# Optimization experiments

Measured on AMD Instinct MI355X. Metric: run time of the kernel, lower is better.

Reference implementation:

```python
import jax, jax.numpy as jnp
import numpy as np

Q_MAX = 127.0          # 2**(8-1) - 1
QUANTILE = 0.99
GAMMA_MIN, GAMMA_MAX = 0.1, 10.0


def setup_inputs() -> dict:
    key = jax.random.key(0)
    k1, _ = jax.random.split(key)
    x = jax.random.normal(k1, (4, 4096, 2048), dtype=jnp.float32)
    gamma = jnp.ones((1,), dtype=jnp.float32)
    return {"x": x, "gamma": gamma}


def reference(x, gamma):
    # --- quantile of |x| (torch: x.flatten().abs().sort().values[k]) ---
    n = x.size
    k = int(round(QUANTILE * n))
    x_abs = jnp.abs(x.ravel())
    # faithful to full-sort-then-index (the kernel-headroom target)
    q_quantile = jax.lax.stop_gradient(jnp.sort(x_abs)[k])

    # first call: buffer initialized to q_quantile, then EMA with itself
    # -> effective running quantile == q_quantile on this step.
    gamma_c = jnp.clip(gamma, GAMMA_MIN, GAMMA_MAX)  # in-place data clamp in torch
    scale = (q_quantile / Q_MAX) * gamma_c            # shape (1,)

    # omniquant: affine fake-quantize with straight-through estimator
    xq = jnp.clip(jnp.round(x / scale), -Q_MAX - 1.0, Q_MAX) * scale
    out = x + jax.lax.stop_gradient(xq - x)           # STE
    return out
```

## Files before the change

### kernel.cpp

```cpp
#include <hip/hip_runtime.h>
#include <math.h>

typedef unsigned int u32;
typedef unsigned long long u64;
typedef float nfloat4 __attribute__((ext_vector_type(4)));

#define AL(p) __hip_atomic_load((p), __ATOMIC_RELAXED, __HIP_MEMORY_SCOPE_AGENT)


#define G1 0
#define SC 2048
#define TK 2056
#define CS 2060
#define H2 4096
#define ZERO_U32 (4096 + (1 << 20))

__global__ __launch_bounds__(1024) void hist_top(const u32* __restrict__ x,
                                                 u32* __restrict__ ws,
                                                 long long n, u32 k) {
  u32* g1 = ws + G1;
  u32* sc = ws + SC;
  __shared__ u32 h[2048 * 8];
  const int t = threadIdx.x;
  for (int i = t; i < 2048 * 8; i += 1024) h[i] = 0;
  __syncthreads();

  const u32 r = (u32)(t & 7);
  const long long n4 = n >> 2;
  const long long stride = (long long)gridDim.x * 1024;
  const uint4* x4 = (const uint4*)x;
  for (long long i = (long long)blockIdx.x * 1024 + t; i < n4; i += stride) {
    uint4 v = x4[i];
    atomicAdd(&h[(((v.x & 0x7fffffffu) >> 20) << 3) + r], 1u);
    atomicAdd(&h[(((v.y & 0x7fffffffu) >> 20) << 3) + r], 1u);
    atomicAdd(&h[(((v.z & 0x7fffffffu) >> 20) << 3) + r], 1u);
    atomicAdd(&h[(((v.w & 0x7fffffffu) >> 20) << 3) + r], 1u);
  }
  for (long long i = (n4 << 2) + (long long)blockIdx.x * 1024 + t; i < n;
       i += stride)
    atomicAdd(&h[(((x[i] & 0x7fffffffu) >> 20) << 3) + r], 1u);
  __syncthreads();
  for (int i = t; i < 2048; i += 1024) {
    u32 c = 0;
#pragma unroll
    for (int j = 0; j < 8; ++j) c += h[(i << 3) + j];
    if (c) atomicAdd(&g1[i], c);
  }
  __syncthreads();
  __shared__ u32 isLast;
  if (t == 0) {
    u32 done = __hip_atomic_fetch_add(ws + TK, 1u, __ATOMIC_ACQ_REL,
                                      __HIP_MEMORY_SCOPE_AGENT);
    isLast = (done == (u32)(gridDim.x - 1));
  }
  __syncthreads();
  if (!isLast) return;
  u32* s = h;
  const u32 c0 = AL(&g1[2 * t]);
  const u32 c1 = AL(&g1[2 * t + 1]);
  const u32 sum = c0 + c1;
  s[t] = sum;
  __syncthreads();
  for (int off = 1; off < 1024; off <<= 1) {
    u32 add = (t >= off) ? s[t - off] : 0u;
    __syncthreads();
    s[t] += add;
    __syncthreads();
  }
  u32 ex = s[t] - sum;
  if (k >= ex && k < ex + c0) { sc[0] = 2 * t; sc[1] = k - ex; }
  ex += c0;
  if (k >= ex && k < ex + c1) { sc[0] = 2 * t + 1; sc[1] = k - ex; }
}

__global__ __launch_bounds__(1024) void hist_low(const u32* __restrict__ x,
                                                 u32* __restrict__ ws,
                                                 long long n) {
  const u32 B1 = ws[SC + 0];
  u32* h2 = ws + H2;
  const int t = threadIdx.x;
  const long long n4 = n >> 2;
  const long long stride = (long long)gridDim.x * 1024;
  const uint4* x4 = (const uint4*)x;
  for (long long i = (long long)blockIdx.x * 1024 + t; i < n4; i += stride) {
    uint4 v = x4[i];
    u32 a;
    a = v.x & 0x7fffffffu; if ((a >> 20) == B1) atomicAdd(&h2[a & 0xFFFFFu], 1u);
    a = v.y & 0x7fffffffu; if ((a >> 20) == B1) atomicAdd(&h2[a & 0xFFFFFu], 1u);
    a = v.z & 0x7fffffffu; if ((a >> 20) == B1) atomicAdd(&h2[a & 0xFFFFFu], 1u);
    a = v.w & 0x7fffffffu; if ((a >> 20) == B1) atomicAdd(&h2[a & 0xFFFFFu], 1u);
  }
  for (long long i = (n4 << 2) + (long long)blockIdx.x * 1024 + t; i < n;
       i += stride) {
    u32 a = x[i] & 0x7fffffffu;
    if ((a >> 20) == B1) atomicAdd(&h2[a & 0xFFFFFu], 1u);
  }
}

__global__ __launch_bounds__(256) void chunk_fin(u32* __restrict__ ws,
                                                 const float* __restrict__ gamma) {
  const u32* h2 = ws + H2;
  u32* cs = ws + CS;
  u32* sc = ws + SC;
  const int t = threadIdx.x;
  const int b = blockIdx.x;
  uint4 v = ((const uint4*)(h2 + (size_t)b * 1024))[t];
  u32 sum = v.x + v.y + v.z + v.w;
#pragma unroll
  for (int off = 32; off > 0; off >>= 1) sum += __shfl_down(sum, off, 64);
  __shared__ u32 w[4];
  if ((t & 63) == 0) w[t >> 6] = sum;
  __syncthreads();
  __shared__ u32 isLast;
  if (t == 0) {
    const u32 total = w[0] + w[1] + w[2] + w[3];
    if (total) atomicAdd(&cs[b], total);
    u32 done = __hip_atomic_fetch_add(ws + TK + 1, 1u, __ATOMIC_ACQ_REL,
                                      __HIP_MEMORY_SCOPE_AGENT);
    isLast = (done == (u32)(gridDim.x - 1));
  }
  __syncthreads();
  if (!isLast) return;
  __shared__ u32 s[256];
  __shared__ u32 sChunk, sK2;
  const u32 k1 = sc[1];
  u32 c[4];
#pragma unroll
  for (int j = 0; j < 4; ++j) c[j] = AL(&cs[4 * t + j]);
  u32 mySum = c[0] + c[1] + c[2] + c[3];
  s[t] = mySum;
  __syncthreads();
  for (int off = 1; off < 256; off <<= 1) {
    u32 add = (t >= off) ? s[t - off] : 0u;
    __syncthreads();
    s[t] += add;
    __syncthreads();
  }
  u32 ex = s[t] - mySum;
#pragma unroll
  for (int j = 0; j < 4; ++j) {
    if (k1 >= ex && k1 < ex + c[j]) {
      sChunk = (u32)(4 * t + j);
      sK2 = k1 - ex;
    }
    ex += c[j];
  }
  __syncthreads();
  const u32 csel = sChunk;
  const u32 k2 = sK2;
  u32 c2[4];
#pragma unroll
  for (int j = 0; j < 4; ++j) c2[j] = h2[(size_t)csel * 1024 + 4 * t + j];
  mySum = c2[0] + c2[1] + c2[2] + c2[3];
  __syncthreads();
  s[t] = mySum;
  __syncthreads();
  for (int off = 1; off < 256; off <<= 1) {
    u32 add = (t >= off) ? s[t - off] : 0u;
    __syncthreads();
    s[t] += add;
    __syncthreads();
  }
  ex = s[t] - mySum;
#pragma unroll
  for (int j = 0; j < 4; ++j) {
    if (k2 >= ex && k2 < ex + c2[j]) {
      const u32 bits = (sc[0] << 20) | (csel * 1024u + (u32)(4 * t + j));
      const float q = __uint_as_float(bits);
      float gm = gamma[0];
      gm = fminf(fmaxf(gm, 0.1f), 10.0f);
      sc[4] = __float_as_uint((q / 127.0f) * gm);
    }
    ex += c2[j];
  }
}

__global__ __launch_bounds__(256) void quantize(const float* __restrict__ x,
                                                float* __restrict__ out,
                                                const u32* __restrict__ ws,
                                                long long n) {
  const float scale = __uint_as_float(ws[SC + 4]);
  const long long n4 = n >> 2;
  const long long stride = (long long)gridDim.x * 256;
  const float4* x4 = (const float4*)x;
  nfloat4* o4 = (nfloat4*)out;
  for (long long i = (long long)blockIdx.x * 256 + threadIdx.x; i < n4;
       i += stride) {
    float4 v = x4[i];
    nfloat4 o;
    o.x = fminf(fmaxf(rintf(v.x / scale), -128.0f), 127.0f) * scale;
    o.y = fminf(fmaxf(rintf(v.y / scale), -128.0f), 127.0f) * scale;
    o.z = fminf(fmaxf(rintf(v.z / scale), -128.0f), 127.0f) * scale;
    o.w = fminf(fmaxf(rintf(v.w / scale), -128.0f), 127.0f) * scale;
    __builtin_nontemporal_store(o, &o4[i]);
  }
  for (long long i = (n4 << 2) + (long long)blockIdx.x * 256 + threadIdx.x;
       i < n; i += stride) {
    float v = x[i];
    out[i] = fminf(fmaxf(rintf(v / scale), -128.0f), 127.0f) * scale;
  }
}

extern "C" void kernel_launch(void* const* d_in, const int* in_sizes, int n_in,
                              void* d_out, int out_size, void* d_ws,
                              size_t ws_size, hipStream_t stream) {
  const u32* xbits = (const u32*)d_in[0];
  const float* gamma = (const float*)d_in[1];
  const long long n = (long long)in_sizes[0];
  u32* ws = (u32*)d_ws;

  const u32 k = (u32)llround(0.99 * (double)n);

  (void)hipMemsetAsync(ws, 0, (size_t)ZERO_U32 * sizeof(u32), stream);
  hist_top<<<512, 1024, 0, stream>>>(xbits, ws, n, k);
  hist_low<<<512, 1024, 0, stream>>>(xbits, ws, n);
  chunk_fin<<<1024, 256, 0, stream>>>(ws, gamma);
  quantize<<<2048, 256, 0, stream>>>((const float*)d_in[0], (float*)d_out, ws,
                                     n);
}
```

Measured before the change: 318.2 us.

## Replace last-block atomic tickets with redundant per-block scans in consumer kernels

```diff
diff --git a/kernel.cpp b/kernel.cpp
--- a/kernel.cpp
+++ b/kernel.cpp
@@ -2,24 +2,18 @@
 #include <math.h>
 
 typedef unsigned int u32;
-typedef unsigned long long u64;
 typedef float nfloat4 __attribute__((ext_vector_type(4)));
 
-#define AL(p) __hip_atomic_load((p), __ATOMIC_RELAXED, __HIP_MEMORY_SCOPE_AGENT)
-
 
 #define G1 0
-#define SC 2048
-#define TK 2056
-#define CS 2060
+#define CS 2048
 #define H2 4096
 #define ZERO_U32 (4096 + (1 << 20))
 
 __global__ __launch_bounds__(1024) void hist_top(const u32* __restrict__ x,
                                                  u32* __restrict__ ws,
-                                                 long long n, u32 k) {
+                                                 long long n) {
   u32* g1 = ws + G1;
-  u32* sc = ws + SC;
   __shared__ u32 h[2048 * 8];
   const int t = threadIdx.x;
   for (int i = t; i < 2048 * 8; i += 1024) h[i] = 0;
@@ -46,39 +40,35 @@
     for (int j = 0; j < 8; ++j) c += h[(i << 3) + j];
     if (c) atomicAdd(&g1[i], c);
   }
-  __syncthreads();
-  __shared__ u32 isLast;
-  if (t == 0) {
-    u32 done = __hip_atomic_fetch_add(ws + TK, 1u, __ATOMIC_ACQ_REL,
-                                      __HIP_MEMORY_SCOPE_AGENT);
-    isLast = (done == (u32)(gridDim.x - 1));
-  }
-  __syncthreads();
-  if (!isLast) return;
-  u32* s = h;
-  const u32 c0 = AL(&g1[2 * t]);
-  const u32 c1 = AL(&g1[2 * t + 1]);
-  const u32 sum = c0 + c1;
-  s[t] = sum;
-  __syncthreads();
-  for (int off = 1; off < 1024; off <<= 1) {
-    u32 add = (t >= off) ? s[t - off] : 0u;
-    __syncthreads();
-    s[t] += add;
-    __syncthreads();
-  }
-  u32 ex = s[t] - sum;
-  if (k >= ex && k < ex + c0) { sc[0] = 2 * t; sc[1] = k - ex; }
-  ex += c0;
-  if (k >= ex && k < ex + c1) { sc[0] = 2 * t + 1; sc[1] = k - ex; }
 }
 
 __global__ __launch_bounds__(1024) void hist_low(const u32* __restrict__ x,
                                                  u32* __restrict__ ws,
-                                                 long long n) {
-  const u32 B1 = ws[SC + 0];
+                                                 long long n, u32 k) {
+  __shared__ u32 s[1024];
+  __shared__ u32 resB1;
+  const u32* g1 = ws + G1;
   u32* h2 = ws + H2;
   const int t = threadIdx.x;
+  {
+    const uint2 c2 = ((const uint2*)g1)[t];
+    const u32 sum = c2.x + c2.y;
+    s[t] = sum;
+    __syncthreads();
+    for (int off = 1; off < 1024; off <<= 1) {
+      u32 add = (t >= off) ? s[t - off] : 0u;
+      __syncthreads();
+      s[t] += add;
+      __syncthreads();
+    }
+    u32 ex = s[t] - sum;
+    if (k >= ex && k < ex + c2.x) resB1 = 2 * t;
+    ex += c2.x;
+    if (k >= ex && k < ex + c2.y) resB1 = 2 * t + 1;
+    __syncthreads();
+  }
+  const u32 B1 = resB1;
+
   const long long n4 = n >> 2;
   const long long stride = (long long)gridDim.x * 1024;
   const uint4* x4 = (const uint4*)x;
@@ -97,95 +87,115 @@
   }
 }
 
-__global__ __launch_bounds__(256) void chunk_fin(u32* __restrict__ ws,
-                                                 const float* __restrict__ gamma) {
+__global__ __launch_bounds__(256) void chunk_reduce(u32* __restrict__ ws) {
   const u32* h2 = ws + H2;
   u32* cs = ws + CS;
-  u32* sc = ws + SC;
-  const int t = threadIdx.x;
-  const int b = blockIdx.x;
-  uint4 v = ((const uint4*)(h2 + (size_t)b * 1024))[t];
+  const int t = threadIdx.x;
+  uint4 v = ((const uint4*)(h2 + (size_t)blockIdx.x * 1024))[t];
   u32 sum = v.x + v.y + v.z + v.w;
 #pragma unroll
   for (int off = 32; off > 0; off >>= 1) sum += __shfl_down(sum, off, 64);
   __shared__ u32 w[4];
   if ((t & 63) == 0) w[t >> 6] = sum;
   __syncthreads();
-  __shared__ u32 isLast;
-  if (t == 0) {
-    const u32 total = w[0] + w[1] + w[2] + w[3];
-    if (total) atomicAdd(&cs[b], total);
-    u32 done = __hip_atomic_fetch_add(ws + TK + 1, 1u, __ATOMIC_ACQ_REL,
-                                      __HIP_MEMORY_SCOPE_AGENT);
-    isLast = (done == (u32)(gridDim.x - 1));
-  }
-  __syncthreads();
-  if (!isLast) return;
-  __shared__ u32 s[256];
-  __shared__ u32 sChunk, sK2;
-  const u32 k1 = sc[1];
-  u32 c[4];
-#pragma unroll
-  for (int j = 0; j < 4; ++j) c[j] = AL(&cs[4 * t + j]);
-  u32 mySum = c[0] + c[1] + c[2] + c[3];
-  s[t] = mySum;
-  __syncthreads();
-  for (int off = 1; off < 256; off <<= 1) {
-    u32 add = (t >= off) ? s[t - off] : 0u;
-    __syncthreads();
-    s[t] += add;
-    __syncthreads();
-  }
-  u32 ex = s[t] - mySum;
-#pragma unroll
-  for (int j = 0; j < 4; ++j) {
-    if (k1 >= ex && k1 < ex + c[j]) {
-      sChunk = (u32)(4 * t + j);
-      sK2 = k1 - ex;
-    }
-    ex += c[j];
-  }
-  __syncthreads();
-  const u32 csel = sChunk;
-  const u32 k2 = sK2;
-  u32 c2[4];
-#pragma unroll
-  for (int j = 0; j < 4; ++j) c2[j] = h2[(size_t)csel * 1024 + 4 * t + j];
-  mySum = c2[0] + c2[1] + c2[2] + c2[3];
-  __syncthreads();
-  s[t] = mySum;
-  __syncthreads();
-  for (int off = 1; off < 256; off <<= 1) {
-    u32 add = (t >= off) ? s[t - off] : 0u;
-    __syncthreads();
-    s[t] += add;
-    __syncthreads();
-  }
-  ex = s[t] - mySum;
-#pragma unroll
-  for (int j = 0; j < 4; ++j) {
-    if (k2 >= ex && k2 < ex + c2[j]) {
-      const u32 bits = (sc[0] << 20) | (csel * 1024u + (u32)(4 * t + j));
-      const float q = __uint_as_float(bits);
-      float gm = gamma[0];
-      gm = fminf(fmaxf(gm, 0.1f), 10.0f);
-      sc[4] = __float_as_uint((q / 127.0f) * gm);
-    }
-    ex += c2[j];
-  }
+  if (t == 0) cs[blockIdx.x] = w[0] + w[1] + w[2] + w[3];
 }
 
 __global__ __launch_bounds__(256) void quantize(const float* __restrict__ x,
                                                 float* __restrict__ out,
                                                 const u32* __restrict__ ws,
-                                                long long n) {
-  const float scale = __uint_as_float(ws[SC + 4]);
+                                                const float* __restrict__ gamma,
+                                                long long n, u32 k) {
+  __shared__ u32 s[256];
+  __shared__ u32 r0, r1;
+  __shared__ float fscale;
+  const u32* g1 = ws + G1;
+  const u32* cs = ws + CS;
+  const u32* h2 = ws + H2;
+  const int t = threadIdx.x;
+
+  u32 B1, k1;
+  {
+    u32 c[8], sum = 0;
+#pragma unroll
+    for (int j = 0; j < 8; ++j) { c[j] = g1[t * 8 + j]; sum += c[j]; }
+    s[t] = sum;
+    __syncthreads();
+    for (int off = 1; off < 256; off <<= 1) {
+      u32 add = (t >= off) ? s[t - off] : 0u;
+      __syncthreads();
+      s[t] += add;
+      __syncthreads();
+    }
+    u32 ex = s[t] - sum;
+#pragma unroll
+    for (int j = 0; j < 8; ++j) {
+      if (k >= ex && k < ex + c[j]) { r0 = (u32)(t * 8 + j); r1 = k - ex; }
+      ex += c[j];
+    }
+    __syncthreads();
+    B1 = r0; k1 = r1;
+  }
+  u32 chunk, k2;
+  {
+    u32 c[4], sum = 0;
+#pragma unroll
+    for (int j = 0; j < 4; ++j) { c[j] = cs[t * 4 + j]; sum += c[j]; }
+    __syncthreads();
+    s[t] = sum;
+    __syncthreads();
+    for (int off = 1; off < 256; off <<= 1) {
+      u32 add = (t >= off) ? s[t - off] : 0u;
+      __syncthreads();
+      s[t] += add;
+      __syncthreads();
+    }
+    u32 ex = s[t] - sum;
+#pragma unroll
+    for (int j = 0; j < 4; ++j) {
+      if (k1 >= ex && k1 < ex + c[j]) { r0 = (u32)(t * 4 + j); r1 = k1 - ex; }
+      ex += c[j];
+    }
+    __syncthreads();
+    chunk = r0; k2 = r1;
+  }
+  {
+    u32 c[4], sum = 0;
+#pragma unroll
+    for (int j = 0; j < 4; ++j) {
+      c[j] = h2[(size_t)chunk * 1024 + t * 4 + j];
+      sum += c[j];
+    }
+    __syncthreads();
+    s[t] = sum;
+    __syncthreads();
+    for (int off = 1; off < 256; off <<= 1) {
+      u32 add = (t >= off) ? s[t - off] : 0u;
+      __syncthreads();
+      s[t] += add;
+      __syncthreads();
+    }
+    u32 ex = s[t] - sum;
+#pragma unroll
+    for (int j = 0; j < 4; ++j) {
+      if (k2 >= ex && k2 < ex + c[j]) {
+        const u32 bits = (B1 << 20) | (chunk * 1024u + (u32)(t * 4 + j));
+        const float q = __uint_as_float(bits);
+        float gm = gamma[0];
+        gm = fminf(fmaxf(gm, 0.1f), 10.0f);
+        fscale = (q / 127.0f) * gm;
+      }
+      ex += c[j];
+    }
+    __syncthreads();
+  }
+  const float scale = fscale;
+
   const long long n4 = n >> 2;
   const long long stride = (long long)gridDim.x * 256;
   const float4* x4 = (const float4*)x;
   nfloat4* o4 = (nfloat4*)out;
-  for (long long i = (long long)blockIdx.x * 256 + threadIdx.x; i < n4;
-       i += stride) {
+  for (long long i = (long long)blockIdx.x * 256 + t; i < n4; i += stride) {
     float4 v = x4[i];
     nfloat4 o;
     o.x = fminf(fmaxf(rintf(v.x / scale), -128.0f), 127.0f) * scale;
@@ -194,8 +204,8 @@
     o.w = fminf(fmaxf(rintf(v.w / scale), -128.0f), 127.0f) * scale;
     __builtin_nontemporal_store(o, &o4[i]);
   }
-  for (long long i = (n4 << 2) + (long long)blockIdx.x * 256 + threadIdx.x;
-       i < n; i += stride) {
+  for (long long i = (n4 << 2) + (long long)blockIdx.x * 256 + t; i < n;
+       i += stride) {
     float v = x[i];
     out[i] = fminf(fmaxf(rintf(v / scale), -128.0f), 127.0f) * scale;
   }
@@ -212,9 +222,9 @@
   const u32 k = (u32)llround(0.99 * (double)n);
 
   (void)hipMemsetAsync(ws, 0, (size_t)ZERO_U32 * sizeof(u32), stream);
-  hist_top<<<512, 1024, 0, stream>>>(xbits, ws, n, k);
-  hist_low<<<512, 1024, 0, stream>>>(xbits, ws, n);
-  chunk_fin<<<1024, 256, 0, stream>>>(ws, gamma);
+  hist_top<<<512, 1024, 0, stream>>>(xbits, ws, n);
+  hist_low<<<512, 1024, 0, stream>>>(xbits, ws, n, k);
+  chunk_reduce<<<1024, 256, 0, stream>>>(ws);
   quantize<<<2048, 256, 0, stream>>>((const float*)d_in[0], (float*)d_out, ws,
-                                     n);
-}
+                                     gamma, n, k);
+}
```

Measured after the change: 282.0 us. 1.13x faster.
